# Kernel tuning notes

Hardware: AMD Instinct MI355X
Metric: run time of the kernel (lower is better)

## Reference

```python
import jax, jax.numpy as jnp
import numpy as np

B, IN_DIM, D, P = 256, 1024, 512, 2048


def setup_inputs() -> dict:
    key = jax.random.key(0)
    ks = jax.random.split(key, 7)
    return {
        "x": jax.random.normal(ks[0], (B, IN_DIM), dtype=jnp.float32),
        "y": jax.random.randint(ks[1], (B,), 0, P),
        "Wb": jax.random.normal(ks[2], (D, IN_DIM), dtype=jnp.float32) * 0.02,
        "bb": jax.random.normal(ks[3], (D,), dtype=jnp.float32) * 0.02,
        "Wm": jax.random.normal(ks[4], (P, D), dtype=jnp.float32) * 0.02,
        "bm": jax.random.normal(ks[5], (P,), dtype=jnp.float32) * 0.02,
        "proxies": jax.random.normal(ks[6], (P, D), dtype=jnp.float32),
    }


def reference(x, y, Wb, bb, Wm, bm, proxies):
    # backbone: Linear(in_dim -> D)
    feat = x @ Wb.T + bb                         # [B, D]
    # L2-norm regularizer: mean of per-row L2 norms
    reg_e = jnp.mean(jnp.sqrt(jnp.sum(feat * feat, axis=1)))
    # multi: classification head Linear(D -> P)
    out = feat @ Wm.T + bm                       # [B, P]
    # squared euclidean distance to each proxy (broadcast diff + square + sum)
    den = jnp.sum((feat[:, None, :] - proxies[None, :, :]) ** 2, axis=2)  # [B, P]
    # cross-entropy on negated distances
    logp = jax.nn.log_softmax(-den, axis=1)      # [B, P]
    loss = -jnp.mean(jnp.take_along_axis(logp, y[:, None], axis=1))
    return out, loss, reg_e
```

## Files before the change

kernel.cpp:

```cpp
#include <hip/hip_runtime.h>
#include <math.h>

#define NB   256
#define KIN  1024
#define ND   512
#define NP   2048
#define NTOT 4096

typedef __bf16 bf16x8 __attribute__((ext_vector_type(8)));
typedef float  f32x4  __attribute__((ext_vector_type(4)));
typedef unsigned short ush8 __attribute__((ext_vector_type(8)));

#define OFF_XB     0u
#define OFF_WBB    524288u
#define OFF_WPB    1572864u
#define OFF_FEATB  5767168u
#define OFF_PN2    6029312u
#define OFF_LOGITS 6037504u
#define OFF_ROWLP  8134656u
#define OFF_ROWNM  8135680u

__device__ __forceinline__ unsigned short f2bf(float f) {
    union { float f; unsigned u; } v; v.f = f;
    unsigned r = v.u + 0x7fffu + ((v.u >> 16) & 1u);
    return (unsigned short)(r >> 16);
}
__device__ __forceinline__ float bf2f(unsigned short h) {
    union { unsigned u; float f; } v; v.u = ((unsigned)h) << 16; return v.f;
}

template <int KDIM, int KSTEPS>
__device__ __forceinline__ void mfma_core(
    const unsigned short* __restrict__ A, const unsigned short* __restrict__ B,
    int m0, int n0, unsigned short* As, unsigned short* Bs, f32x4 (&acc)[2][2])
{
    const int t = threadIdx.x;
    const int lane = t & 63, w = t >> 6;
    const int wm = (w >> 1) * 32, wn = (w & 1) * 32;
    const int srow = t >> 2, sc = (t & 3) * 8;
    const unsigned short* ga = A + (size_t)(m0 + srow) * KDIM + sc;
    const unsigned short* gb = B + (size_t)(n0 + srow) * KDIM + sc;
    const int arow = wm + (lane & 15), brow = wn + (lane & 15);
    const int fcol = (lane >> 4) * 8;

    for (int ks = 0; ks < KSTEPS; ++ks) {
        ush8 va = *(const ush8*)(ga + ks * 32);
        ush8 vb = *(const ush8*)(gb + ks * 32);
        __syncthreads();
        *(ush8*)&As[srow * 32 + sc] = va;
        *(ush8*)&Bs[srow * 32 + sc] = vb;
        __syncthreads();
        bf16x8 af0 = *(const bf16x8*)&As[(arow     ) * 32 + fcol];
        bf16x8 af1 = *(const bf16x8*)&As[(arow + 16) * 32 + fcol];
        bf16x8 bf0 = *(const bf16x8*)&Bs[(brow     ) * 32 + fcol];
        bf16x8 bf1 = *(const bf16x8*)&Bs[(brow + 16) * 32 + fcol];
        acc[0][0] = __builtin_amdgcn_mfma_f32_16x16x32_bf16(af0, bf0, acc[0][0], 0, 0, 0);
        acc[0][1] = __builtin_amdgcn_mfma_f32_16x16x32_bf16(af0, bf1, acc[0][1], 0, 0, 0);
        acc[1][0] = __builtin_amdgcn_mfma_f32_16x16x32_bf16(af1, bf0, acc[1][0], 0, 0, 0);
        acc[1][1] = __builtin_amdgcn_mfma_f32_16x16x32_bf16(af1, bf1, acc[1][1], 0, 0, 0);
    }
}

__global__ __launch_bounds__(256) void k_prep(
    const float* __restrict__ x, const float* __restrict__ Wb,
    const float* __restrict__ Wm, const float* __restrict__ prox,
    unsigned short* __restrict__ xb, unsigned short* __restrict__ Wbb,
    unsigned short* __restrict__ WPb, float* __restrict__ pn2)
{
    const int bid = blockIdx.x, t = threadIdx.x;
    const float* src; unsigned short* dst; int b;
    if (bid < 128)       { src = x;    dst = xb;  b = bid; }
    else if (bid < 384)  { src = Wb;   dst = Wbb; b = bid - 128; }
    else if (bid < 896)  { src = Wm;   dst = WPb; b = bid - 384; }
    else if (bid < 1408) { src = prox; dst = WPb + (size_t)NP * ND; b = bid - 896; }
    else {
        const int wave = t >> 6, lane = t & 63;
        const int row = (bid - 1408) * 4 + wave;
        const float* pr = prox + (size_t)row * ND + lane * 8;
        float4 v0 = *(const float4*)pr;
        float4 v1 = *(const float4*)(pr + 4);
        float s = v0.x*v0.x + v0.y*v0.y + v0.z*v0.z + v0.w*v0.w
                + v1.x*v1.x + v1.y*v1.y + v1.z*v1.z + v1.w*v1.w;
#pragma unroll
        for (int off = 32; off; off >>= 1) s += __shfl_down(s, off);
        if (lane == 0) pn2[row] = s;
        return;
    }
    const int idx = (b * 256 + t) * 8;
    float4 f0 = *(const float4*)(src + idx);
    float4 f1 = *(const float4*)(src + idx + 4);
    ush8 o;
    o[0] = f2bf(f0.x); o[1] = f2bf(f0.y); o[2] = f2bf(f0.z); o[3] = f2bf(f0.w);
    o[4] = f2bf(f1.x); o[5] = f2bf(f1.y); o[6] = f2bf(f1.z); o[7] = f2bf(f1.w);
    *(ush8*)(dst + idx) = o;
}

__global__ __launch_bounds__(256) void k_feat(
    const unsigned short* __restrict__ xb, const unsigned short* __restrict__ Wbb,
    const float* __restrict__ bb, unsigned short* __restrict__ featb)
{
    __shared__ unsigned short As[64 * 32];
    __shared__ unsigned short Bs[64 * 32];
    const int n0 = blockIdx.x * 64;
    const int m0 = blockIdx.y * 64;
    f32x4 acc[2][2] = {};
    mfma_core<KIN, KIN / 32>(xb, Wbb, m0, n0, As, Bs, acc);
    const int lane = threadIdx.x & 63, w = threadIdx.x >> 6;
    const int wm = (w >> 1) * 32, wn = (w & 1) * 32;
    const int q = lane >> 4, cn = lane & 15;
#pragma unroll
    for (int i = 0; i < 2; ++i)
#pragma unroll
        for (int j = 0; j < 2; ++j) {
            const int n = n0 + wn + 16 * j + cn;
            const float bias = bb[n];
#pragma unroll
            for (int r = 0; r < 4; ++r) {
                const int m = m0 + wm + 16 * i + q * 4 + r;
                featb[m * ND + n] = f2bf(acc[i][j][r] + bias);
            }
        }
}

__global__ __launch_bounds__(256) void k_head(
    const unsigned short* __restrict__ featb, const unsigned short* __restrict__ WPb,
    const float* __restrict__ bm, const float* __restrict__ pn2,
    float* __restrict__ out, float* __restrict__ logits)
{
    __shared__ unsigned short As[64 * 32];
    __shared__ unsigned short Bs[64 * 32];
    const int n0 = blockIdx.x * 64;
    const int m0 = blockIdx.y * 64;
    f32x4 acc[2][2] = {};
    mfma_core<ND, ND / 32>(featb, WPb, m0, n0, As, Bs, acc);
    const int lane = threadIdx.x & 63, w = threadIdx.x >> 6;
    const int wm = (w >> 1) * 32, wn = (w & 1) * 32;
    const int q = lane >> 4, cn = lane & 15;
    const bool isProxy = (n0 >= NP);
#pragma unroll
    for (int i = 0; i < 2; ++i)
#pragma unroll
        for (int j = 0; j < 2; ++j) {
            const int n = n0 + wn + 16 * j + cn;
            const float cadd = isProxy ? pn2[n - NP] : bm[n];
#pragma unroll
            for (int r = 0; r < 4; ++r) {
                const int m = m0 + wm + 16 * i + q * 4 + r;
                const float v = acc[i][j][r];
                if (isProxy) logits[m * NP + (n - NP)] = 2.0f * v - cadd;
                else         out[m * NP + n] = v + cadd;
            }
        }
}

__device__ __forceinline__ float block_reduce(float v, float* sred, int op)
{
    const int lane = threadIdx.x & 63, wave = threadIdx.x >> 6;
#pragma unroll
    for (int off = 32; off; off >>= 1) {
        float o = __shfl_down(v, off);
        v = op ? fmaxf(v, o) : (v + o);
    }
    if (lane == 0) sred[wave] = v;
    __syncthreads();
    if (threadIdx.x == 0) {
        float r = sred[0];
#pragma unroll
        for (int wv = 1; wv < 4; ++wv) r = op ? fmaxf(r, sred[wv]) : (r + sred[wv]);
        sred[0] = r;
    }
    __syncthreads();
    float r = sred[0];
    __syncthreads();
    return r;
}

__global__ __launch_bounds__(256) void k_loss(
    const unsigned short* __restrict__ featb, const float* __restrict__ logits,
    const int* __restrict__ y, float* __restrict__ rowlp, float* __restrict__ rownm)
{
    __shared__ float sred[4];
    const int b = blockIdx.x, t = threadIdx.x;

    float s = 0.f;
#pragma unroll
    for (int c = 0; c < 2; ++c) {
        float v = bf2f(featb[b * ND + t * 2 + c]); s += v * v;
    }
    float fn2 = block_reduce(s, sred, 0);

    const float* lr = logits + (size_t)b * NP;
    float lv[8], mx = -INFINITY;
#pragma unroll
    for (int j = 0; j < 8; ++j) { lv[j] = lr[t + 256 * j]; mx = fmaxf(mx, lv[j]); }
    float MX = block_reduce(mx, sred, 1);
    float es = 0.f;
#pragma unroll
    for (int j = 0; j < 8; ++j) es += __expf(lv[j] - MX);
    float SUM = block_reduce(es, sred, 0);

    if (t == 0) {
        float ly = lr[y[b]];
        rowlp[b] = ly - MX - __logf(SUM);
        rownm[b] = sqrtf(fn2);
    }
}

__global__ __launch_bounds__(256) void k_final(
    const float* __restrict__ rowlp, const float* __restrict__ rownm,
    float* __restrict__ tail)
{
    __shared__ float sred[4];
    const int t = threadIdx.x;
    float s1 = block_reduce(rowlp[t], sred, 0);
    float s2 = block_reduce(rownm[t], sred, 0);
    if (t == 0) {
        tail[0] = -s1 / (float)NB;
        tail[1] =  s2 / (float)NB;
    }
}

extern "C" void kernel_launch(void* const* d_in, const int* in_sizes, int n_in,
                              void* d_out, int out_size, void* d_ws, size_t ws_size,
                              hipStream_t stream)
{
    const float* x       = (const float*)d_in[0];
    const int*   y       = (const int*)  d_in[1];
    const float* Wb      = (const float*)d_in[2];
    const float* bb      = (const float*)d_in[3];
    const float* Wm      = (const float*)d_in[4];
    const float* bm      = (const float*)d_in[5];
    const float* proxies = (const float*)d_in[6];

    char* ws = (char*)d_ws;
    unsigned short* xb     = (unsigned short*)(ws + OFF_XB);
    unsigned short* Wbb    = (unsigned short*)(ws + OFF_WBB);
    unsigned short* WPb    = (unsigned short*)(ws + OFF_WPB);
    unsigned short* featb  = (unsigned short*)(ws + OFF_FEATB);
    float*          pn2    = (float*)(ws + OFF_PN2);
    float*          logits = (float*)(ws + OFF_LOGITS);
    float*          rowlp  = (float*)(ws + OFF_ROWLP);
    float*          rownm  = (float*)(ws + OFF_ROWNM);

    float* out  = (float*)d_out;
    float* tail = out + (size_t)NB * NP;

    k_prep<<<dim3(1920), dim3(256), 0, stream>>>(x, Wb, Wm, proxies, xb, Wbb, WPb, pn2);
    k_feat<<<dim3(ND / 64, NB / 64), dim3(256), 0, stream>>>(xb, Wbb, bb, featb);
    k_head<<<dim3(NTOT / 64, NB / 64), dim3(256), 0, stream>>>(featb, WPb, bm, pn2, out, logits);
    k_loss<<<dim3(NB), dim3(256), 0, stream>>>(featb, logits, y, rowlp, rownm);
    k_final<<<dim3(1), dim3(256), 0, stream>>>(rowlp, rownm, tail);
}
```

Measured before the change: 99.79 us.

## Fuse conversion into feature GEMM and enlarge head tiles with async LDS loads

Merges the bf16 prep kernel and the feature GEMM into one launch. The feature GEMM now reads fp32 x and Wb directly, converts them in registers and double-buffers LDS with a register prefetch, so the bf16 copies of x and Wb are no longer written. The head GEMM moves to 128x128 tiles with a 4x4 MFMA block per wave and double-buffered direct global-to-LDS loads. This raises data reuse but cuts the head grid to 64 blocks, which may leave most CUs idle. Proxy norms are now computed from the same loads used for the bf16 conversion.

```diff
diff --git a/kernel.cpp b/kernel.cpp
--- a/kernel.cpp
+++ b/kernel.cpp
@@ -1,4 +1,5 @@
 #include <hip/hip_runtime.h>
+#include <hip/hip_bf16.h>
 #include <math.h>
 
 #define NB   256
@@ -11,115 +12,102 @@
 typedef float  f32x4  __attribute__((ext_vector_type(4)));
 typedef unsigned short ush8 __attribute__((ext_vector_type(8)));
 
-#define OFF_XB     0u
-#define OFF_WBB    524288u
-#define OFF_WPB    1572864u
-#define OFF_FEATB  5767168u
-#define OFF_PN2    6029312u
-#define OFF_LOGITS 6037504u
-#define OFF_ROWLP  8134656u
-#define OFF_ROWNM  8135680u
-
-__device__ __forceinline__ unsigned short f2bf(float f) {
-    union { float f; unsigned u; } v; v.f = f;
-    unsigned r = v.u + 0x7fffu + ((v.u >> 16) & 1u);
-    return (unsigned short)(r >> 16);
-}
+#define OFF_WPB    0u
+#define OFF_FEATB  4194304u
+#define OFF_PN2    4456448u
+#define OFF_LOGITS 4464640u
+#define OFF_ROWLP  6561792u
+#define OFF_ROWNM  6562816u
+
 __device__ __forceinline__ float bf2f(unsigned short h) {
     union { unsigned u; float f; } v; v.u = ((unsigned)h) << 16; return v.f;
 }
 
-template <int KDIM, int KSTEPS>
-__device__ __forceinline__ void mfma_core(
-    const unsigned short* __restrict__ A, const unsigned short* __restrict__ B,
-    int m0, int n0, unsigned short* As, unsigned short* Bs, f32x4 (&acc)[2][2])
-{
-    const int t = threadIdx.x;
+__device__ __forceinline__ ush8 pack8(float4 f0, float4 f1) {
+    union { ush8 v; __hip_bfloat162 h[4]; } o;
+    o.h[0] = __float22bfloat162_rn(make_float2(f0.x, f0.y));
+    o.h[1] = __float22bfloat162_rn(make_float2(f0.z, f0.w));
+    o.h[2] = __float22bfloat162_rn(make_float2(f1.x, f1.y));
+    o.h[3] = __float22bfloat162_rn(make_float2(f1.z, f1.w));
+    return o.v;
+}
+
+__device__ __forceinline__ void async16(const unsigned short* g, unsigned short* l) {
+    __builtin_amdgcn_global_load_lds(
+        (const __attribute__((address_space(1))) unsigned int*)g,
+        (__attribute__((address_space(3))) unsigned int*)l, 16, 0, 0);
+}
+
+__global__ __launch_bounds__(256) void k_one(
+    const float* __restrict__ x, const float* __restrict__ Wb,
+    const float* __restrict__ bb, const float* __restrict__ Wm,
+    const float* __restrict__ prox, unsigned short* __restrict__ featb,
+    unsigned short* __restrict__ WPb, float* __restrict__ pn2)
+{
+    const int bid = blockIdx.x, t = threadIdx.x;
     const int lane = t & 63, w = t >> 6;
-    const int wm = (w >> 1) * 32, wn = (w & 1) * 32;
-    const int srow = t >> 2, sc = (t & 3) * 8;
-    const unsigned short* ga = A + (size_t)(m0 + srow) * KDIM + sc;
-    const unsigned short* gb = B + (size_t)(n0 + srow) * KDIM + sc;
-    const int arow = wm + (lane & 15), brow = wn + (lane & 15);
-    const int fcol = (lane >> 4) * 8;
-
-    for (int ks = 0; ks < KSTEPS; ++ks) {
-        ush8 va = *(const ush8*)(ga + ks * 32);
-        ush8 vb = *(const ush8*)(gb + ks * 32);
-        __syncthreads();
-        *(ush8*)&As[srow * 32 + sc] = va;
-        *(ush8*)&Bs[srow * 32 + sc] = vb;
-        __syncthreads();
-        bf16x8 af0 = *(const bf16x8*)&As[(arow     ) * 32 + fcol];
-        bf16x8 af1 = *(const bf16x8*)&As[(arow + 16) * 32 + fcol];
-        bf16x8 bf0 = *(const bf16x8*)&Bs[(brow     ) * 32 + fcol];
-        bf16x8 bf1 = *(const bf16x8*)&Bs[(brow + 16) * 32 + fcol];
-        acc[0][0] = __builtin_amdgcn_mfma_f32_16x16x32_bf16(af0, bf0, acc[0][0], 0, 0, 0);
-        acc[0][1] = __builtin_amdgcn_mfma_f32_16x16x32_bf16(af0, bf1, acc[0][1], 0, 0, 0);
-        acc[1][0] = __builtin_amdgcn_mfma_f32_16x16x32_bf16(af1, bf0, acc[1][0], 0, 0, 0);
-        acc[1][1] = __builtin_amdgcn_mfma_f32_16x16x32_bf16(af1, bf1, acc[1][1], 0, 0, 0);
-    }
-}
-
-__global__ __launch_bounds__(256) void k_prep(
-    const float* __restrict__ x, const float* __restrict__ Wb,
-    const float* __restrict__ Wm, const float* __restrict__ prox,
-    unsigned short* __restrict__ xb, unsigned short* __restrict__ Wbb,
-    unsigned short* __restrict__ WPb, float* __restrict__ pn2)
-{
-    const int bid = blockIdx.x, t = threadIdx.x;
-    const float* src; unsigned short* dst; int b;
-    if (bid < 128)       { src = x;    dst = xb;  b = bid; }
-    else if (bid < 384)  { src = Wb;   dst = Wbb; b = bid - 128; }
-    else if (bid < 896)  { src = Wm;   dst = WPb; b = bid - 384; }
-    else if (bid < 1408) { src = prox; dst = WPb + (size_t)NP * ND; b = bid - 896; }
-    else {
-        const int wave = t >> 6, lane = t & 63;
-        const int row = (bid - 1408) * 4 + wave;
-        const float* pr = prox + (size_t)row * ND + lane * 8;
-        float4 v0 = *(const float4*)pr;
-        float4 v1 = *(const float4*)(pr + 4);
-        float s = v0.x*v0.x + v0.y*v0.y + v0.z*v0.z + v0.w*v0.w
-                + v1.x*v1.x + v1.y*v1.y + v1.z*v1.z + v1.w*v1.w;
+    if (bid < 32) {
+        __shared__ unsigned short As[2][64 * 32];
+        __shared__ unsigned short Bs[2][64 * 32];
+        const int n0 = (bid & 7) * 64, m0 = (bid >> 3) * 64;
+        const int srow = t >> 2, sc = (t & 3) * 8;
+        const float* gA = x  + (size_t)(m0 + srow) * KIN + sc;
+        const float* gB = Wb + (size_t)(n0 + srow) * KIN + sc;
+        float4 a0 = *(const float4*)gA, a1 = *(const float4*)(gA + 4);
+        float4 b0 = *(const float4*)gB, b1 = *(const float4*)(gB + 4);
+        f32x4 acc[2][2] = {};
+        const int wm = (w >> 1) * 32, wn = (w & 1) * 32;
+        const int arow = wm + (lane & 15), brow = wn + (lane & 15);
+        const int fcol = (lane >> 4) * 8;
+        for (int ks = 0; ks < KIN / 32; ++ks) {
+            *(ush8*)&As[ks & 1][srow * 32 + sc] = pack8(a0, a1);
+            *(ush8*)&Bs[ks & 1][srow * 32 + sc] = pack8(b0, b1);
+            __syncthreads();
+            if (ks + 1 < KIN / 32) {
+                a0 = *(const float4*)(gA + (ks + 1) * 32);
+                a1 = *(const float4*)(gA + (ks + 1) * 32 + 4);
+                b0 = *(const float4*)(gB + (ks + 1) * 32);
+                b1 = *(const float4*)(gB + (ks + 1) * 32 + 4);
+            }
+            const unsigned short* as = &As[ks & 1][0];
+            const unsigned short* bs = &Bs[ks & 1][0];
+            bf16x8 af0 = *(const bf16x8*)&as[(arow     ) * 32 + fcol];
+            bf16x8 af1 = *(const bf16x8*)&as[(arow + 16) * 32 + fcol];
+            bf16x8 bf0 = *(const bf16x8*)&bs[(brow     ) * 32 + fcol];
+            bf16x8 bf1 = *(const bf16x8*)&bs[(brow + 16) * 32 + fcol];
+            acc[0][0] = __builtin_amdgcn_mfma_f32_16x16x32_bf16(af0, bf0, acc[0][0], 0, 0, 0);
+            acc[0][1] = __builtin_amdgcn_mfma_f32_16x16x32_bf16(af0, bf1, acc[0][1], 0, 0, 0);
+            acc[1][0] = __builtin_amdgcn_mfma_f32_16x16x32_bf16(af1, bf0, acc[1][0], 0, 0, 0);
+            acc[1][1] = __builtin_amdgcn_mfma_f32_16x16x32_bf16(af1, bf1, acc[1][1], 0, 0, 0);
+        }
+        const int q = lane >> 4, cn = lane & 15;
+#pragma unroll
+        for (int i = 0; i < 2; ++i)
+#pragma unroll
+            for (int j = 0; j < 2; ++j) {
+                const int n = n0 + wn + 16 * j + cn;
+                const float bias = bb[n];
+#pragma unroll
+                for (int r = 0; r < 4; ++r) {
+                    const int m = m0 + wm + 16 * i + q * 4 + r;
+                    featb[m * ND + n] = __hip_bfloat16_raw(__hip_bfloat16(acc[i][j][r] + bias)).x;
+                }
+            }
+    } else if (bid < 544) {
+        const int idx = (bid - 32) * 2048 + t * 8;
+        float4 f0 = *(const float4*)(Wm + idx), f1 = *(const float4*)(Wm + idx + 4);
+        *(ush8*)(WPb + idx) = pack8(f0, f1);
+    } else {
+        const int b = bid - 544;
+        const int idx = b * 2048 + t * 8;
+        float4 f0 = *(const float4*)(prox + idx), f1 = *(const float4*)(prox + idx + 4);
+        *(ush8*)(WPb + (size_t)NP * ND + idx) = pack8(f0, f1);
+        float s = f0.x*f0.x + f0.y*f0.y + f0.z*f0.z + f0.w*f0.w
+                + f1.x*f1.x + f1.y*f1.y + f1.z*f1.z + f1.w*f1.w;
 #pragma unroll
         for (int off = 32; off; off >>= 1) s += __shfl_down(s, off);
-        if (lane == 0) pn2[row] = s;
-        return;
-    }
-    const int idx = (b * 256 + t) * 8;
-    float4 f0 = *(const float4*)(src + idx);
-    float4 f1 = *(const float4*)(src + idx + 4);
-    ush8 o;
-    o[0] = f2bf(f0.x); o[1] = f2bf(f0.y); o[2] = f2bf(f0.z); o[3] = f2bf(f0.w);
-    o[4] = f2bf(f1.x); o[5] = f2bf(f1.y); o[6] = f2bf(f1.z); o[7] = f2bf(f1.w);
-    *(ush8*)(dst + idx) = o;
-}
-
-__global__ __launch_bounds__(256) void k_feat(
-    const unsigned short* __restrict__ xb, const unsigned short* __restrict__ Wbb,
-    const float* __restrict__ bb, unsigned short* __restrict__ featb)
-{
-    __shared__ unsigned short As[64 * 32];
-    __shared__ unsigned short Bs[64 * 32];
-    const int n0 = blockIdx.x * 64;
-    const int m0 = blockIdx.y * 64;
-    f32x4 acc[2][2] = {};
-    mfma_core<KIN, KIN / 32>(xb, Wbb, m0, n0, As, Bs, acc);
-    const int lane = threadIdx.x & 63, w = threadIdx.x >> 6;
-    const int wm = (w >> 1) * 32, wn = (w & 1) * 32;
-    const int q = lane >> 4, cn = lane & 15;
-#pragma unroll
-    for (int i = 0; i < 2; ++i)
-#pragma unroll
-        for (int j = 0; j < 2; ++j) {
-            const int n = n0 + wn + 16 * j + cn;
-            const float bias = bb[n];
-#pragma unroll
-            for (int r = 0; r < 4; ++r) {
-                const int m = m0 + wm + 16 * i + q * 4 + r;
-                featb[m * ND + n] = f2bf(acc[i][j][r] + bias);
-            }
-        }
+        if (lane == 0) pn2[b * 4 + w] = s;
+    }
 }
 
 __global__ __launch_bounds__(256) void k_head(
@@ -127,21 +115,54 @@
     const float* __restrict__ bm, const float* __restrict__ pn2,
     float* __restrict__ out, float* __restrict__ logits)
 {
-    __shared__ unsigned short As[64 * 32];
-    __shared__ unsigned short Bs[64 * 32];
-    const int n0 = blockIdx.x * 64;
-    const int m0 = blockIdx.y * 64;
-    f32x4 acc[2][2] = {};
-    mfma_core<ND, ND / 32>(featb, WPb, m0, n0, As, Bs, acc);
-    const int lane = threadIdx.x & 63, w = threadIdx.x >> 6;
-    const int wm = (w >> 1) * 32, wn = (w & 1) * 32;
-    const int q = lane >> 4, cn = lane & 15;
+    __shared__ unsigned short As[2][128 * 32];
+    __shared__ unsigned short Bs[2][128 * 32];
+    const int t = threadIdx.x, lane = t & 63, w = t >> 6;
+    const int n0 = blockIdx.x * 128;
+    const int m0 = blockIdx.y * 128;
+    const int drow = w * 16 + (lane >> 2), dcol = (lane & 3) * 8;
+    const unsigned short* gA0 = featb + (size_t)(m0 +      drow) * ND + dcol;
+    const unsigned short* gA1 = featb + (size_t)(m0 + 64 + drow) * ND + dcol;
+    const unsigned short* gB0 = WPb   + (size_t)(n0 +      drow) * ND + dcol;
+    const unsigned short* gB1 = WPb   + (size_t)(n0 + 64 + drow) * ND + dcol;
+
+#define ISSUE(buf, ks)                                              \
+    do {                                                            \
+        const int o_ = (ks) * 32;                                   \
+        async16(gA0 + o_, &As[buf][(     w * 16) * 32]);            \
+        async16(gA1 + o_, &As[buf][(64 + w * 16) * 32]);            \
+        async16(gB0 + o_, &Bs[buf][(     w * 16) * 32]);            \
+        async16(gB1 + o_, &Bs[buf][(64 + w * 16) * 32]);            \
+    } while (0)
+
+    f32x4 acc[4][4] = {};
+    const int wm = (w >> 1) * 64, wn = (w & 1) * 64;
+    const int fr = lane & 15, fcol = (lane >> 4) * 8;
+    ISSUE(0, 0);
+    for (int ks = 0; ks < ND / 32; ++ks) {
+        __syncthreads();
+        if (ks + 1 < ND / 32) ISSUE((ks + 1) & 1, ks + 1);
+        const unsigned short* as = &As[ks & 1][0];
+        const unsigned short* bs = &Bs[ks & 1][0];
+        bf16x8 af[4], bf[4];
+#pragma unroll
+        for (int i = 0; i < 4; ++i) af[i] = *(const bf16x8*)&as[(wm + 16 * i + fr) * 32 + fcol];
+#pragma unroll
+        for (int j = 0; j < 4; ++j) bf[j] = *(const bf16x8*)&bs[(wn + 16 * j + fr) * 32 + fcol];
+#pragma unroll
+        for (int i = 0; i < 4; ++i)
+#pragma unroll
+            for (int j = 0; j < 4; ++j)
+                acc[i][j] = __builtin_amdgcn_mfma_f32_16x16x32_bf16(af[i], bf[j], acc[i][j], 0, 0, 0);
+    }
+#undef ISSUE
     const bool isProxy = (n0 >= NP);
-#pragma unroll
-    for (int i = 0; i < 2; ++i)
-#pragma unroll
-        for (int j = 0; j < 2; ++j) {
-            const int n = n0 + wn + 16 * j + cn;
+    const int q = lane >> 4;
+#pragma unroll
+    for (int i = 0; i < 4; ++i)
+#pragma unroll
+        for (int j = 0; j < 4; ++j) {
+            const int n = n0 + wn + 16 * j + fr;
             const float cadd = isProxy ? pn2[n - NP] : bm[n];
 #pragma unroll
             for (int r = 0; r < 4; ++r) {
@@ -233,8 +254,6 @@
     const float* proxies = (const float*)d_in[6];
 
     char* ws = (char*)d_ws;
-    unsigned short* xb     = (unsigned short*)(ws + OFF_XB);
-    unsigned short* Wbb    = (unsigned short*)(ws + OFF_WBB);
     unsigned short* WPb    = (unsigned short*)(ws + OFF_WPB);
     unsigned short* featb  = (unsigned short*)(ws + OFF_FEATB);
     float*          pn2    = (float*)(ws + OFF_PN2);
@@ -245,9 +264,8 @@
     float* out  = (float*)d_out;
     float* tail = out + (size_t)NB * NP;
 
-    k_prep<<<dim3(1920), dim3(256), 0, stream>>>(x, Wb, Wm, proxies, xb, Wbb, WPb, pn2);
-    k_feat<<<dim3(ND / 64, NB / 64), dim3(256), 0, stream>>>(xb, Wbb, bb, featb);
-    k_head<<<dim3(NTOT / 64, NB / 64), dim3(256), 0, stream>>>(featb, WPb, bm, pn2, out, logits);
+    k_one <<<dim3(1056), dim3(256), 0, stream>>>(x, Wb, bb, Wm, proxies, featb, WPb, pn2);
+    k_head<<<dim3(NTOT / 128, NB / 128), dim3(256), 0, stream>>>(featb, WPb, bm, pn2, out, logits);
     k_loss<<<dim3(NB), dim3(256), 0, stream>>>(featb, logits, y, rowlp, rownm);
     k_final<<<dim3(1), dim3(256), 0, stream>>>(rowlp, rownm, tail);
 }
```

Result: slower. 112.3 us (+12.5%).
